# Kernel optimization log

Hardware: AMD Instinct MI355X
Metric: run time of the kernel (lower is better)

Reference implementation:

```python
import jax, jax.numpy as jnp
import numpy as np

N, K = 256, 133
INPUT_W, INPUT_H = 256, 256
SPLIT = 2.0
W = round(INPUT_W * SPLIT)  # 512
H = round(INPUT_H * SPLIT)  # 512
SIGMA = (5.66, 5.66)
BETA = 10.0
LABEL_BETA = 10.0


def setup_inputs() -> dict:
    key = jax.random.key(0)
    k1, k2, k3 = jax.random.split(key, 3)
    pred = jax.random.normal(k1, (N, K, W + H), dtype=jnp.float32)
    xy = jax.random.uniform(k2, (N, K, 2), dtype=jnp.float32) * INPUT_W
    vis = (jax.random.uniform(k3, (N, K, 1), dtype=jnp.float32) > 0.2).astype(jnp.float32)
    keypoints = jnp.concatenate([xy, vis], axis=-1)
    return {"pred": pred, "keypoints": keypoints}


def _gaussian_targets(keypoints):
    # Vectorized equivalent of the Python (n,k) loop in gaussian_smoothng.
    kp_xy = keypoints[..., :2]
    vis = keypoints[..., 2]
    mu = jnp.round(kp_xy * SPLIT)  # int64 in torch; rounded float is numerically identical
    rx = SIGMA[0] * 3.0
    ry = SIGMA[1] * 3.0
    left = mu[..., 0] - rx
    right = mu[..., 0] + rx + 1.0
    top = mu[..., 1] - ry
    bottom = mu[..., 1] + ry + 1.0
    oob = (left >= W) | (top >= H) | (right < 0) | (bottom < 0)
    visible = vis >= 0.5
    valid = visible & (~oob)
    x = jnp.arange(W, dtype=jnp.float32)
    y = jnp.arange(H, dtype=jnp.float32)
    gx = jnp.exp(-((x[None, None, :] - mu[..., 0:1]) ** 2) / (2.0 * SIGMA[0] ** 2))
    gy = jnp.exp(-((y[None, None, :] - mu[..., 1:2]) ** 2) / (2.0 * SIGMA[1] ** 2))
    target_x = jnp.where(valid[..., None], gx, 0.0)  # (N,K,W)
    target_y = jnp.where(valid[..., None], gy, 0.0)  # (N,K,H)
    # weight = visible value, zeroed if visible but out of bounds
    weight = jnp.where(visible & oob, 0.0, vis)
    return target_x, target_y, weight


def _criterion(p, t):
    # p, t: (N*K, L). KLDivLoss(reduction='none') then mean over dim=1.
    log_pt = jax.nn.log_softmax(p * BETA, axis=1)
    lab = jax.nn.softmax(t * LABEL_BETA, axis=1)  # strictly positive
    kl = lab * (jnp.log(lab) - log_pt)
    return kl.mean(axis=1)


def reference(pred, keypoints):
    n, k, _ = pred.shape
    split = pred.shape[-1] // 2
    pred_x = pred[..., :split].reshape(-1, split)
    pred_y = pred[..., split:].reshape(-1, pred.shape[-1] - split)
    gt_x, gt_y, w = _gaussian_targets(keypoints)
    w = w.reshape(-1)
    loss_x = (_criterion(pred_x, gt_x.reshape(-1, W)) * w).sum()
    loss_y = (_criterion(pred_y, gt_y.reshape(-1, H)) * w).sum()
    return (loss_x + loss_y) / k
```

## Files before the change

kernel.cpp:

```cpp
#include <hip/hip_runtime.h>
#include <math.h>

#define NKP 133
#define NROWS (256 * NKP)
#define RH_TOTAL (2 * NROWS)
#define NBLOCKS 2048
#define NWAVES (NBLOCKS * 4)
#define C2P  14.4269504088896f
#define NK2  0.02251706f
#define RAD  16.98f
#define LN2f 0.69314718055994531f

static __device__ __forceinline__ float fexp2(float x) {
    return __builtin_amdgcn_exp2f(x);
}

__global__ __launch_bounds__(256) void rtmcc_partial_kernel(
    const float* __restrict__ pred,
    const float* __restrict__ keypoints,
    float* __restrict__ partials)
{
    const int wave = threadIdx.x >> 6;
    const int lane = threadIdx.x & 63;
    __shared__ float t_em1[256];
    __shared__ float t_eg [256];
    __shared__ float lds[4];

    {
        const int t = threadIdx.x;
        const float d = (float)(t - 128);
        float em1 = 0.0f, eg = 0.0f;
        if (fabsf(d) <= 35.0f) {
            const float g = fexp2(-d * d * NK2);
            const float e = fexp2(g * C2P);
            em1 = e - 1.0f;
            eg  = e * g;
        }
        t_em1[t] = em1;
        t_eg [t] = eg;
    }
    __syncthreads();

    float acc = 0.0f;

    const int rh0 = blockIdx.x * 4 + wave;
    {
        const int r0 = rh0 >> 1;
        float kx = keypoints[r0 * 3 + 0];
        float ky = keypoints[r0 * 3 + 1];
        float kv = keypoints[r0 * 3 + 2];

        for (int rh = rh0; rh < RH_TOTAL; rh += NWAVES) {
            const float kxc = kx, kyc = ky, kvc = kv;
            const int rhn = rh + NWAVES;
            if (rhn < RH_TOTAL) {
                const int rn = rhn >> 1;
                kx = keypoints[rn * 3 + 0];
                ky = keypoints[rn * 3 + 1];
                kv = keypoints[rn * 3 + 2];
            }

            const float mux = rintf(kxc * 2.0f);
            const float muy = rintf(kyc * 2.0f);
            const bool oob = (mux - RAD >= 512.0f) || (muy - RAD >= 512.0f) ||
                             (mux + RAD + 1.0f < 0.0f) || (muy + RAD + 1.0f < 0.0f);
            const bool visible = (kvc >= 0.5f);
            const float w = (visible && oob) ? 0.0f : kvc;
            if (!(w > 0.0f)) continue;
            const bool valid = visible && !oob;

            const float mu  = (rh & 1) ? muy : mux;
            const int   mui = (int)mu;
            const float* pr = pred + (size_t)rh * 512;

            const float* p = pr + lane * 8;
            const float4 pa = *reinterpret_cast<const float4*>(p);
            const float4 pb = *reinterpret_cast<const float4*>(p + 4);
            const float pv[8] = {pa.x, pa.y, pa.z, pa.w, pb.x, pb.y, pb.z, pb.w};

            float S = 0.0f, R = 0.0f;
            #pragma unroll
            for (int u = 0; u < 8; ++u) {
                S += fexp2(C2P * pv[u]);
                R -= pv[u];
            }

            float Zw = 0.0f;
            if (valid) {
                int ws = mui - 64;
                ws = ws < 0 ? 0 : (ws > 384 ? 384 : ws);
                const float pw0 = pr[ws + lane];
                const float pw1 = pr[ws + 64 + lane];
                int t0 = ws + lane - mui + 128;
                int t1 = t0 + 64;
                t0 = t0 > 255 ? 255 : t0;
                t1 = t1 > 255 ? 255 : t1;
                const float em10 = t_em1[t0], eg0 = t_eg[t0];
                const float em11 = t_em1[t1], eg1 = t_eg[t1];
                Zw = em10 + em11;
                R += (eg0 - em10 * pw0) + (eg1 - em11 * pw1);
            }

            #pragma unroll
            for (int off = 1; off < 64; off <<= 1) {
                S  += __shfl_xor(S,  off, 64);
                Zw += __shfl_xor(Zw, off, 64);
                R  += __shfl_xor(R,  off, 64);
            }

            const float Z = 512.0f + Zw;
            const float loss = 10.0f * R / Z + (__log2f(S) - __log2f(Z)) * LN2f;
            acc += w * loss;
        }
    }

    acc *= (1.0f / (512.0f * 133.0f));
    if (lane == 0) lds[wave] = acc;
    __syncthreads();
    if (threadIdx.x == 0)
        partials[blockIdx.x] = lds[0] + lds[1] + lds[2] + lds[3];
}

__global__ __launch_bounds__(256) void rtmcc_reduce_kernel(
    const float* __restrict__ partials, float* __restrict__ out)
{
    __shared__ float lds[4];
    float s = 0.0f;
    for (int i = threadIdx.x; i < NBLOCKS; i += 256) s += partials[i];
    #pragma unroll
    for (int off = 1; off < 64; off <<= 1) s += __shfl_xor(s, off, 64);
    if ((threadIdx.x & 63) == 0) lds[threadIdx.x >> 6] = s;
    __syncthreads();
    if (threadIdx.x == 0) out[0] = lds[0] + lds[1] + lds[2] + lds[3];
}

extern "C" void kernel_launch(void* const* d_in, const int* in_sizes, int n_in,
                              void* d_out, int out_size, void* d_ws, size_t ws_size,
                              hipStream_t stream) {
    const float* pred = (const float*)d_in[0];
    const float* kpts = (const float*)d_in[1];
    float* out = (float*)d_out;
    float* partials = (float*)d_ws;

    rtmcc_partial_kernel<<<NBLOCKS, 256, 0, stream>>>(pred, kpts, partials);
    rtmcc_reduce_kernel<<<1, 256, 0, stream>>>(partials, out);
}
```

Before: 29.31 us.

## Process both row halves per wave and fuse final reduction via last-block atomic

Each wave now handles a whole keypoint row, with each half-wave covering the x or y half using 16 elements per lane. This removes the duplicate keypoint decode and the 64-wide shuffle per half-row. The separate reduce kernel is replaced by a last-block-done atomic counter, reset by a memset before the launch, and the division is swapped for a fast reciprocal. The window now uses four loads per lane to cover the 128-wide window. The memset adds a launch, and the visible-but-in-bounds check is now folded into w.

```diff
diff --git a/kernel.cpp b/kernel.cpp
--- a/kernel.cpp
+++ b/kernel.cpp
@@ -3,7 +3,6 @@
 
 #define NKP 133
 #define NROWS (256 * NKP)
-#define RH_TOTAL (2 * NROWS)
 #define NBLOCKS 2048
 #define NWAVES (NBLOCKS * 4)
 #define C2P  14.4269504088896f
@@ -11,20 +10,24 @@
 #define RAD  16.98f
 #define LN2f 0.69314718055994531f
 
-static __device__ __forceinline__ float fexp2(float x) {
-    return __builtin_amdgcn_exp2f(x);
-}
+static __device__ __forceinline__ float fexp2(float x) { return __builtin_amdgcn_exp2f(x); }
+static __device__ __forceinline__ float frcp (float x) { return __builtin_amdgcn_rcpf(x); }
 
-__global__ __launch_bounds__(256) void rtmcc_partial_kernel(
+__global__ __launch_bounds__(256) void rtmcc_kernel(
     const float* __restrict__ pred,
     const float* __restrict__ keypoints,
-    float* __restrict__ partials)
+    float* __restrict__ partials,
+    unsigned int* __restrict__ counter,
+    float* __restrict__ out)
 {
     const int wave = threadIdx.x >> 6;
     const int lane = threadIdx.x & 63;
+    const int l5   = lane & 31;
+    const int hgrp = lane >> 5;
     __shared__ float t_em1[256];
     __shared__ float t_eg [256];
     __shared__ float lds[4];
+    __shared__ int   is_last;
 
     {
         const int t = threadIdx.x;
@@ -33,105 +36,107 @@
         if (fabsf(d) <= 35.0f) {
             const float g = fexp2(-d * d * NK2);
             const float e = fexp2(g * C2P);
-            em1 = e - 1.0f;
-            eg  = e * g;
+            em1 = e - 1.0f; eg = e * g;
         }
-        t_em1[t] = em1;
-        t_eg [t] = eg;
+        t_em1[t] = em1; t_eg[t] = eg;
     }
     __syncthreads();
 
     float acc = 0.0f;
+    const int wid = blockIdx.x * 4 + wave;
 
-    const int rh0 = blockIdx.x * 4 + wave;
-    {
-        const int r0 = rh0 >> 1;
-        float kx = keypoints[r0 * 3 + 0];
-        float ky = keypoints[r0 * 3 + 1];
-        float kv = keypoints[r0 * 3 + 2];
+    float kx = keypoints[wid * 3 + 0];
+    float ky = keypoints[wid * 3 + 1];
+    float kv = keypoints[wid * 3 + 2];
 
-        for (int rh = rh0; rh < RH_TOTAL; rh += NWAVES) {
-            const float kxc = kx, kyc = ky, kvc = kv;
-            const int rhn = rh + NWAVES;
-            if (rhn < RH_TOTAL) {
-                const int rn = rhn >> 1;
-                kx = keypoints[rn * 3 + 0];
-                ky = keypoints[rn * 3 + 1];
-                kv = keypoints[rn * 3 + 2];
+    for (int row = wid; row < NROWS; row += NWAVES) {
+        const float kxc = kx, kyc = ky, kvc = kv;
+        const int rn = row + NWAVES;
+        if (rn < NROWS) {
+            kx = keypoints[rn * 3 + 0];
+            ky = keypoints[rn * 3 + 1];
+            kv = keypoints[rn * 3 + 2];
+        }
+
+        const float mux = rintf(kxc * 2.0f);
+        const float muy = rintf(kyc * 2.0f);
+        const bool oob = (mux - RAD >= 512.0f) || (muy - RAD >= 512.0f) ||
+                         (mux + RAD + 1.0f < 0.0f) || (muy + RAD + 1.0f < 0.0f);
+        const bool visible = (kvc >= 0.5f);
+        const float w = (visible && oob) ? 0.0f : kvc;
+        if (!(w > 0.0f)) continue;
+
+        const float mu = hgrp ? muy : mux;
+        const float* ph = pred + (size_t)row * 1024 + hgrp * 512;
+
+        const float* p = ph + l5 * 16;
+        const float4 q0 = *reinterpret_cast<const float4*>(p);
+        const float4 q1 = *reinterpret_cast<const float4*>(p + 4);
+        const float4 q2 = *reinterpret_cast<const float4*>(p + 8);
+        const float4 q3 = *reinterpret_cast<const float4*>(p + 12);
+        const float pv[16] = {q0.x,q0.y,q0.z,q0.w, q1.x,q1.y,q1.z,q1.w,
+                              q2.x,q2.y,q2.z,q2.w, q3.x,q3.y,q3.z,q3.w};
+
+        float S = 0.0f, R = 0.0f;
+        #pragma unroll
+        for (int u = 0; u < 16; ++u) {
+            S += fexp2(C2P * pv[u]);
+            R -= pv[u];
+        }
+
+        float Zw = 0.0f;
+        if (visible) {
+            const int mui = (int)mu;
+            int ws = mui - 64; ws = ws < 0 ? 0 : (ws > 384 ? 384 : ws);
+            #pragma unroll
+            for (int v = 0; v < 4; ++v) {
+                const int idx = ws + l5 + v * 32;
+                const float pw = ph[idx];
+                int t = idx - mui + 128;
+                t = t < 0 ? 0 : (t > 255 ? 255 : t);
+                const float em1 = t_em1[t], eg = t_eg[t];
+                Zw += em1;
+                R  += eg - em1 * pw;
             }
+        }
 
-            const float mux = rintf(kxc * 2.0f);
-            const float muy = rintf(kyc * 2.0f);
-            const bool oob = (mux - RAD >= 512.0f) || (muy - RAD >= 512.0f) ||
-                             (mux + RAD + 1.0f < 0.0f) || (muy + RAD + 1.0f < 0.0f);
-            const bool visible = (kvc >= 0.5f);
-            const float w = (visible && oob) ? 0.0f : kvc;
-            if (!(w > 0.0f)) continue;
-            const bool valid = visible && !oob;
+        #pragma unroll
+        for (int off = 1; off < 32; off <<= 1) {
+            S  += __shfl_xor(S,  off, 64);
+            Zw += __shfl_xor(Zw, off, 64);
+            R  += __shfl_xor(R,  off, 64);
+        }
 
-            const float mu  = (rh & 1) ? muy : mux;
-            const int   mui = (int)mu;
-            const float* pr = pred + (size_t)rh * 512;
-
-            const float* p = pr + lane * 8;
-            const float4 pa = *reinterpret_cast<const float4*>(p);
-            const float4 pb = *reinterpret_cast<const float4*>(p + 4);
-            const float pv[8] = {pa.x, pa.y, pa.z, pa.w, pb.x, pb.y, pb.z, pb.w};
-
-            float S = 0.0f, R = 0.0f;
-            #pragma unroll
-            for (int u = 0; u < 8; ++u) {
-                S += fexp2(C2P * pv[u]);
-                R -= pv[u];
-            }
-
-            float Zw = 0.0f;
-            if (valid) {
-                int ws = mui - 64;
-                ws = ws < 0 ? 0 : (ws > 384 ? 384 : ws);
-                const float pw0 = pr[ws + lane];
-                const float pw1 = pr[ws + 64 + lane];
-                int t0 = ws + lane - mui + 128;
-                int t1 = t0 + 64;
-                t0 = t0 > 255 ? 255 : t0;
-                t1 = t1 > 255 ? 255 : t1;
-                const float em10 = t_em1[t0], eg0 = t_eg[t0];
-                const float em11 = t_em1[t1], eg1 = t_eg[t1];
-                Zw = em10 + em11;
-                R += (eg0 - em10 * pw0) + (eg1 - em11 * pw1);
-            }
-
-            #pragma unroll
-            for (int off = 1; off < 64; off <<= 1) {
-                S  += __shfl_xor(S,  off, 64);
-                Zw += __shfl_xor(Zw, off, 64);
-                R  += __shfl_xor(R,  off, 64);
-            }
-
-            const float Z = 512.0f + Zw;
-            const float loss = 10.0f * R / Z + (__log2f(S) - __log2f(Z)) * LN2f;
-            acc += w * loss;
-        }
+        const float Z = 512.0f + Zw;
+        const float loss = 10.0f * R * frcp(Z) + (__log2f(S) - __log2f(Z)) * LN2f;
+        acc += w * loss;
     }
 
-    acc *= (1.0f / (512.0f * 133.0f));
+    acc *= (1.0f / (32.0f * 512.0f * 133.0f));
+    #pragma unroll
+    for (int off = 1; off < 64; off <<= 1) acc += __shfl_xor(acc, off, 64);
     if (lane == 0) lds[wave] = acc;
     __syncthreads();
-    if (threadIdx.x == 0)
+
+    if (threadIdx.x == 0) {
         partials[blockIdx.x] = lds[0] + lds[1] + lds[2] + lds[3];
-}
+        __threadfence();
+        const unsigned int old = atomicAdd(counter, 1u);
+        is_last = (old == NBLOCKS - 1) ? 1 : 0;
+    }
+    __syncthreads();
 
-__global__ __launch_bounds__(256) void rtmcc_reduce_kernel(
-    const float* __restrict__ partials, float* __restrict__ out)
-{
-    __shared__ float lds[4];
-    float s = 0.0f;
-    for (int i = threadIdx.x; i < NBLOCKS; i += 256) s += partials[i];
-    #pragma unroll
-    for (int off = 1; off < 64; off <<= 1) s += __shfl_xor(s, off, 64);
-    if ((threadIdx.x & 63) == 0) lds[threadIdx.x >> 6] = s;
-    __syncthreads();
-    if (threadIdx.x == 0) out[0] = lds[0] + lds[1] + lds[2] + lds[3];
+    if (is_last) {
+        __threadfence();
+        float s = 0.0f;
+        for (int i = threadIdx.x; i < NBLOCKS; i += 256)
+            s += ((volatile const float*)partials)[i];
+        #pragma unroll
+        for (int off = 1; off < 64; off <<= 1) s += __shfl_xor(s, off, 64);
+        if ((threadIdx.x & 63) == 0) lds[threadIdx.x >> 6] = s;
+        __syncthreads();
+        if (threadIdx.x == 0) out[0] = lds[0] + lds[1] + lds[2] + lds[3];
+    }
 }
 
 extern "C" void kernel_launch(void* const* d_in, const int* in_sizes, int n_in,
@@ -141,7 +146,8 @@
     const float* kpts = (const float*)d_in[1];
     float* out = (float*)d_out;
     float* partials = (float*)d_ws;
+    unsigned int* counter = (unsigned int*)((char*)d_ws + NBLOCKS * sizeof(float));
 
-    rtmcc_partial_kernel<<<NBLOCKS, 256, 0, stream>>>(pred, kpts, partials);
-    rtmcc_reduce_kernel<<<1, 256, 0, stream>>>(partials, out);
+    hipMemsetAsync(counter, 0, sizeof(unsigned int), stream);
+    rtmcc_kernel<<<NBLOCKS, 256, 0, stream>>>(pred, kpts, partials, counter, out);
 }
```

Measured after the change: 83.34 us. 2.84x slower.
